# Performance work log

Hardware: AMD Instinct MI355X
Metric: run time of the kernel (lower is better)

## Reference

```python
import jax, jax.numpy as jnp
import numpy as np

SEQ, BATCH, HIDDEN, HEADS = 2048, 2, 1024, 16
HEAD_DIM = HIDDEN // HEADS
NORM = float(np.sqrt(HEAD_DIM))
NEG_MIN = float(np.finfo(np.float32).min)


def setup_inputs() -> dict:
    key = jax.random.key(0)
    ks = jax.random.split(key, 9)
    xavier = lambda k: (jax.random.normal(k, (HIDDEN, HIDDEN), jnp.float32)
                        * np.sqrt(2.0 / (HIDDEN + HIDDEN)))
    hidden_states = jax.random.normal(ks[0], (SEQ, BATCH, HIDDEN), jnp.float32)
    # causal (left-to-right) bool mask, True = attend
    attention_mask = jnp.tril(jnp.ones((SEQ, SEQ), dtype=bool))[None, None, :, :]
    return {
        "hidden_states": hidden_states,
        "attention_mask": attention_mask,
        "Wq": xavier(ks[1]), "bq": jnp.zeros((HIDDEN,), jnp.float32),
        "Wk": xavier(ks[2]), "bk": jnp.zeros((HIDDEN,), jnp.float32),
        "Wv": xavier(ks[3]), "bv": jnp.zeros((HIDDEN,), jnp.float32),
        "Wo": xavier(ks[4]), "bo": jnp.zeros((HIDDEN,), jnp.float32),
    }


def reference(hidden_states, attention_mask, Wq, bq, Wk, bk, Wv, bv, Wo, bo):
    s, b, _ = hidden_states.shape
    # projections (F.linear: x @ W.T + b), seq-first layout -> [s,b,h,d]
    q = (hidden_states @ Wq.T + bq).reshape(s, b, HEADS, HEAD_DIM) / NORM
    k = (hidden_states @ Wk.T + bk).reshape(s, b, HEADS, HEAD_DIM)
    v = (hidden_states @ Wv.T + bv).reshape(s, b, HEADS, HEAD_DIM)
    # scores [b,h,q,k] (Q already pre-scaled by 1/sqrt(d))
    scores = jnp.einsum("qbhd,kbhd->bhqk", q, k)
    scores = jnp.where(attention_mask, scores, NEG_MIN)
    probs = jax.nn.softmax(scores, axis=-1)
    # context [b,h,q,d] -> permute(2,0,1,3) -> [q,b,h,d] -> [q,b,hidden]
    ctx = jnp.einsum("bhqk,kbhd->qbhd", probs, v).reshape(s, b, HIDDEN)
    return ctx @ Wo.T + bo
```

## Files before the change

kernel.cpp:

```cpp
#include <hip/hip_runtime.h>
#include <hip/hip_bf16.h>
#include <cstdint>
#include <math.h>

#define SEQ 2048
#define BATCH 2
#define HID 1024
#define NH 16
#define HD 64
#define MROWS (SEQ * BATCH)

typedef __attribute__((ext_vector_type(8))) short bf16x8;
typedef __attribute__((ext_vector_type(4))) float f32x4;

typedef const __attribute__((address_space(1))) void* gas_t;
typedef __attribute__((address_space(3))) void* las_t;

static __device__ __forceinline__ unsigned short f2bf(float x) {
    __hip_bfloat16 h = __float2bfloat16(x);
    unsigned short u;
    __builtin_memcpy(&u, &h, 2);
    return u;
}

__global__ __launch_bounds__(256) void f2bf_kern(const float* __restrict__ in,
                                                 unsigned short* __restrict__ out,
                                                 int n8) {
    int i = blockIdx.x * 256 + threadIdx.x;
    if (i >= n8) return;
    const float4* p = (const float4*)in + (size_t)i * 2;
    float4 a = p[0], b = p[1];
    union { unsigned short us[8]; uint4 v; } o;
    o.us[0] = f2bf(a.x); o.us[1] = f2bf(a.y); o.us[2] = f2bf(a.z); o.us[3] = f2bf(a.w);
    o.us[4] = f2bf(b.x); o.us[5] = f2bf(b.y); o.us[6] = f2bf(b.z); o.us[7] = f2bf(b.w);
    ((uint4*)out)[i] = o.v;
}

#define GBK 32

template <int BNT2>
__global__ __launch_bounds__(256) void gemm_bf16(
    const unsigned short* __restrict__ A, const unsigned short* __restrict__ W,
    const float* __restrict__ b0, const float* __restrict__ b1,
    const float* __restrict__ b2,
    unsigned short* __restrict__ Qo, unsigned short* __restrict__ Ko,
    unsigned short* __restrict__ Vo, float* __restrict__ Fo, int mode) {
    constexpr int BN = BNT2 * 32;
    __shared__ unsigned short As[2][128 * GBK];
    __shared__ unsigned short Bs[2][BN * GBK];
    const int t = threadIdx.x;
    const int lane = t & 63, w = t >> 6;
    const int wr = w & 1, wc = w >> 1;
    const int m0 = blockIdx.x * 128, n0 = blockIdx.y * BN;

    f32x4 acc[4][BNT2];
#pragma unroll
    for (int i = 0; i < 4; ++i)
#pragma unroll
        for (int j = 0; j < BNT2; ++j) acc[i][j] = {0.f, 0.f, 0.f, 0.f};

    const unsigned short* gA = A + (size_t)(m0 + w * 16 + (lane >> 2)) * HID + (lane & 3) * 8;
    const unsigned short* gB = W + (size_t)(n0 + w * 16 + (lane >> 2)) * HID + (lane & 3) * 8;

    auto stage = [&](int buf, int k0) {
#pragma unroll
        for (int c = 0; c < 2; ++c)
            __builtin_amdgcn_global_load_lds((gas_t)(gA + (size_t)c * 64 * HID + k0),
                                             (las_t)(&As[buf][(c * 64 + w * 16) * GBK]), 16, 0, 0);
#pragma unroll
        for (int c = 0; c < BN / 64; ++c)
            __builtin_amdgcn_global_load_lds((gas_t)(gB + (size_t)c * 64 * HID + k0),
                                             (las_t)(&Bs[buf][(c * 64 + w * 16) * GBK]), 16, 0, 0);
    };

    const int arow = wr * 64 + (lane & 15);
    const int brow = wc * (BNT2 * 16) + (lane & 15);
    const int kfo = (lane >> 4) * 8;

    stage(0, 0);
    int cur = 0;
    for (int k0 = 0; k0 < HID; k0 += GBK) {
        __syncthreads();
        if (k0 + GBK < HID) stage(cur ^ 1, k0 + GBK);
        bf16x8 af[4], bfr[BNT2];
#pragma unroll
        for (int mt = 0; mt < 4; ++mt)
            af[mt] = *(const bf16x8*)(&As[cur][(arow + mt * 16) * GBK + kfo]);
#pragma unroll
        for (int nt = 0; nt < BNT2; ++nt)
            bfr[nt] = *(const bf16x8*)(&Bs[cur][(brow + nt * 16) * GBK + kfo]);
#pragma unroll
        for (int mt = 0; mt < 4; ++mt)
#pragma unroll
            for (int nt = 0; nt < BNT2; ++nt)
                acc[mt][nt] = __builtin_amdgcn_mfma_f32_16x16x32_bf16(
                    af[mt], bfr[nt], acc[mt][nt], 0, 0, 0);
        cur ^= 1;
    }

    const int seg = n0 >> 10;
    const float* bias = (mode == 1) ? b0 : (seg == 0 ? b0 : (seg == 1 ? b1 : b2));
    const float scale = (mode == 0 && seg == 0) ? 0.125f : 1.0f;
    const int nbase = (n0 & 1023) + wc * (BNT2 * 16);

    float bvals[BNT2];
#pragma unroll
    for (int nt = 0; nt < BNT2; ++nt)
        bvals[nt] = bias[nbase + nt * 16 + (lane & 15)];

#pragma unroll
    for (int mt = 0; mt < 4; ++mt)
#pragma unroll
        for (int nt = 0; nt < BNT2; ++nt)
#pragma unroll
            for (int i = 0; i < 4; ++i) {
                float v = (acc[mt][nt][i] + bvals[nt]) * scale;
                int m = m0 + wr * 64 + mt * 16 + (lane >> 4) * 4 + i;
                int n = nbase + nt * 16 + (lane & 15);
                if (mode == 1) {
                    Fo[(size_t)m * HID + n] = v;
                } else if (seg == 0) {
                    Qo[(size_t)m * HID + n] = f2bf(v);
                } else if (seg == 1) {
                    Ko[(size_t)m * HID + n] = f2bf(v);
                } else {
                    Vo[(size_t)n * MROWS + (m & 1) * SEQ + (m >> 1)] = f2bf(v);
                }
            }
}

__global__ __launch_bounds__(256) void attn_mfma(const unsigned short* __restrict__ Qb,
                                                 const unsigned short* __restrict__ Kb,
                                                 const unsigned short* __restrict__ Vt,
                                                 unsigned short* __restrict__ Ob) {
    __shared__ unsigned short Kl[2][64 * 64];
    __shared__ unsigned short Vl[2][64 * 64];
    __shared__ unsigned short QP[64 * 64];

    const int t = threadIdx.x;
    const int lane = t & 63, w = t >> 6;

    const int flat = (int)blockIdx.x + (int)blockIdx.y * 32;
    const int xcd = flat & 7, ii = flat >> 3;
    const int bh = xcd * 4 + (ii >> 5);
    const int qt = 31 - (ii & 31);
    const int b = bh >> 4, h = bh & 15;
    const int q0 = qt * 64;

    const int lrow_base = w * 8 + (lane >> 3);
    const int chunkb = (lane & 7) * 16;

    auto stage_kv = [&](int buf, int kt) {
        const int k0 = kt * 64;
#pragma unroll
        for (int c = 0; c < 2; ++c) {
            int lr = c * 32 + lrow_base;
            int sb = chunkb ^ ((lr & 7) << 4);
            const unsigned short* ksrc =
                Kb + ((size_t)(k0 + lr) * 2 + b) * HID + h * 64 + (sb >> 1);
            const unsigned short* vsrc =
                Vt + (size_t)(h * 64 + lr) * MROWS + b * SEQ + k0 + (sb >> 1);
            __builtin_amdgcn_global_load_lds((gas_t)ksrc,
                (las_t)(&Kl[buf][(c * 32 + w * 8) * 64]), 16, 0, 0);
            __builtin_amdgcn_global_load_lds((gas_t)vsrc,
                (las_t)(&Vl[buf][(c * 32 + w * 8) * 64]), 16, 0, 0);
        }
    };

    stage_kv(0, 0);

#pragma unroll
    for (int c = 0; c < 2; ++c) {
        int f = c * 256 + t;
        int r = f >> 3, dc = f & 7;
        uint4 v = *(const uint4*)(Qb + (size_t)((q0 + r) * 2 + b) * HID + h * 64 + dc * 8);
        *(uint4*)((char*)QP + r * 128 + ((dc * 16) ^ ((r & 7) << 4))) = v;
    }

    f32x4 acc[4];
#pragma unroll
    for (int nt = 0; nt < 4; ++nt) acc[nt] = {0.f, 0.f, 0.f, 0.f};
    float mrow[4] = {-INFINITY, -INFINITY, -INFINITY, -INFINITY};
    float lrow[4] = {0.f, 0.f, 0.f, 0.f};
    bf16x8 qf[2];

    int cur = 0;
    for (int kt = 0; kt <= qt; ++kt) {
        __syncthreads();
        if (kt < qt) stage_kv(cur ^ 1, kt + 1);
        if (kt == 0) {
            int r = w * 16 + (lane & 15);
            int base = r * 128, sw = (r & 7) << 4;
            qf[0] = *(const bf16x8*)((char*)QP + base + ((((lane >> 4) * 16) + 0) ^ sw));
            qf[1] = *(const bf16x8*)((char*)QP + base + ((((lane >> 4) * 16) + 64) ^ sw));
        }
        const char* Kc = (const char*)Kl[cur];
        const char* Vc = (const char*)Vl[cur];

        f32x4 s[4];
#pragma unroll
        for (int ct = 0; ct < 4; ++ct) {
            int j = ct * 16 + (lane & 15);
            int base = j * 128, sw = (j & 7) << 4;
            bf16x8 kf0 = *(const bf16x8*)(Kc + base + ((((lane >> 4) * 16) + 0) ^ sw));
            bf16x8 kf1 = *(const bf16x8*)(Kc + base + ((((lane >> 4) * 16) + 64) ^ sw));
            f32x4 z = {0.f, 0.f, 0.f, 0.f};
            z = __builtin_amdgcn_mfma_f32_16x16x32_bf16(qf[0], kf0, z, 0, 0, 0);
            z = __builtin_amdgcn_mfma_f32_16x16x32_bf16(qf[1], kf1, z, 0, 0, 0);
            s[ct] = z;
        }

        if (kt == qt) {
#pragma unroll
            for (int ct = 0; ct < 4; ++ct) {
                int j = ct * 16 + (lane & 15);
#pragma unroll
                for (int i = 0; i < 4; ++i) {
                    int q = w * 16 + (lane >> 4) * 4 + i;
                    if (j > q) s[ct][i] = -3.0e38f;
                }
            }
        }

#pragma unroll
        for (int i = 0; i < 4; ++i) {
            float mx = fmaxf(fmaxf(s[0][i], s[1][i]), fmaxf(s[2][i], s[3][i]));
            mx = fmaxf(mx, __shfl_xor(mx, 1));
            mx = fmaxf(mx, __shfl_xor(mx, 2));
            mx = fmaxf(mx, __shfl_xor(mx, 4));
            mx = fmaxf(mx, __shfl_xor(mx, 8));
            float mn = fmaxf(mrow[i], mx);
            float corr = __expf(mrow[i] - mn);
            mrow[i] = mn;
            float rs = 0.f;
#pragma unroll
            for (int ct = 0; ct < 4; ++ct) {
                float pe = __expf(s[ct][i] - mn);
                s[ct][i] = pe;
                rs += pe;
            }
            rs += __shfl_xor(rs, 1);
            rs += __shfl_xor(rs, 2);
            rs += __shfl_xor(rs, 4);
            rs += __shfl_xor(rs, 8);
            lrow[i] = lrow[i] * corr + rs;
#pragma unroll
            for (int nt = 0; nt < 4; ++nt) acc[nt][i] *= corr;
        }

#pragma unroll
        for (int ct = 0; ct < 4; ++ct)
#pragma unroll
            for (int i = 0; i < 4; ++i) {
                int r = w * 16 + (lane >> 4) * 4 + i;
                int jb = (ct * 16 + (lane & 15)) * 2;
                *(unsigned short*)((char*)QP + r * 128 + (jb ^ ((r & 7) << 4))) = f2bf(s[ct][i]);
            }
        asm volatile("s_waitcnt lgkmcnt(0)" ::: "memory");
        __builtin_amdgcn_sched_barrier(0);

        bf16x8 pf[2];
        {
            int r = w * 16 + (lane & 15);
            int base = r * 128, sw = (r & 7) << 4;
            pf[0] = *(const bf16x8*)((char*)QP + base + ((((lane >> 4) * 16) + 0) ^ sw));
            pf[1] = *(const bf16x8*)((char*)QP + base + ((((lane >> 4) * 16) + 64) ^ sw));
        }
#pragma unroll
        for (int nt = 0; nt < 4; ++nt) {
            int d = nt * 16 + (lane & 15);
            int base = d * 128, sw = (d & 7) << 4;
            bf16x8 v0 = *(const bf16x8*)(Vc + base + ((((lane >> 4) * 16) + 0) ^ sw));
            bf16x8 v1 = *(const bf16x8*)(Vc + base + ((((lane >> 4) * 16) + 64) ^ sw));
            acc[nt] = __builtin_amdgcn_mfma_f32_16x16x32_bf16(pf[0], v0, acc[nt], 0, 0, 0);
            acc[nt] = __builtin_amdgcn_mfma_f32_16x16x32_bf16(pf[1], v1, acc[nt], 0, 0, 0);
        }
        cur ^= 1;
    }

#pragma unroll
    for (int i = 0; i < 4; ++i) {
        float inv = 1.0f / lrow[i];
        int q = q0 + w * 16 + (lane >> 4) * 4 + i;
#pragma unroll
        for (int nt = 0; nt < 4; ++nt) {
            int col = h * 64 + nt * 16 + (lane & 15);
            Ob[(size_t)(q * 2 + b) * HID + col] = f2bf(acc[nt][i] * inv);
        }
    }
}

extern "C" void kernel_launch(void* const* d_in, const int* in_sizes, int n_in,
                              void* d_out, int out_size, void* d_ws, size_t ws_size,
                              hipStream_t stream) {
    const float* hs = (const float*)d_in[0];
    const float* Wq = (const float*)d_in[2];
    const float* bq = (const float*)d_in[3];
    const float* Wk = (const float*)d_in[4];
    const float* bk = (const float*)d_in[5];
    const float* Wv = (const float*)d_in[6];
    const float* bv = (const float*)d_in[7];
    const float* Wo = (const float*)d_in[8];
    const float* bo = (const float*)d_in[9];

    char* ws = (char*)d_ws;
    unsigned short* hs_bf   = (unsigned short*)(ws);
    unsigned short* Wqkv_bf = (unsigned short*)(ws + (8u << 20));
    unsigned short* Wo_bf   = (unsigned short*)(ws + (14u << 20));
    unsigned short* Q_bf    = (unsigned short*)(ws + (16u << 20));
    unsigned short* K_bf    = (unsigned short*)(ws + (24u << 20));
    unsigned short* Vt_bf   = (unsigned short*)(ws + (32u << 20));
    unsigned short* ctx_bf  = (unsigned short*)(ws + (40u << 20));

    dim3 blk(256);
    const int WN8 = HID * HID / 8;
    hipLaunchKernelGGL(f2bf_kern, dim3(MROWS * HID / 8 / 256), blk, 0, stream, hs, hs_bf, MROWS * HID / 8);
    hipLaunchKernelGGL(f2bf_kern, dim3(WN8 / 256), blk, 0, stream, Wq, Wqkv_bf, WN8);
    hipLaunchKernelGGL(f2bf_kern, dim3(WN8 / 256), blk, 0, stream, Wk, Wqkv_bf + (size_t)HID * HID, WN8);
    hipLaunchKernelGGL(f2bf_kern, dim3(WN8 / 256), blk, 0, stream, Wv, Wqkv_bf + (size_t)2 * HID * HID, WN8);
    hipLaunchKernelGGL(f2bf_kern, dim3(WN8 / 256), blk, 0, stream, Wo, Wo_bf, WN8);

    hipLaunchKernelGGL((gemm_bf16<4>), dim3(MROWS / 128, 24), blk, 0, stream,
                       hs_bf, Wqkv_bf, bq, bk, bv, Q_bf, K_bf, Vt_bf, (float*)nullptr, 0);

    hipLaunchKernelGGL(attn_mfma, dim3(32, 32), blk, 0, stream,
                       Q_bf, K_bf, Vt_bf, ctx_bf);

    hipLaunchKernelGGL((gemm_bf16<2>), dim3(MROWS / 128, 16), blk, 0, stream,
                       ctx_bf, Wo_bf, bo, bo, bo,
                       (unsigned short*)nullptr, (unsigned short*)nullptr,
                       (unsigned short*)nullptr, (float*)d_out, 1);
}
```

Measured before the change: 274.6 us.

## Triple-buffer GEMM with vmcnt waits, XCD-aware remap, and pair causal attention tiles

The GEMM moves from double to triple buffering with explicit vmcnt waits and raw barriers, so two tiles of loads stay in flight while MFMAs run. Its block index is also remapped so that blocks sharing weight columns land on the same XCD, for better L2 reuse. The attention kernel now gives each block two query tiles (qt and 31-qt), which balances causal work per block and halves the grid. The costs are more LDS per GEMM block and fewer attention blocks, which may lower occupancy and parallelism.

```diff
diff --git a/kernel.cpp b/kernel.cpp
--- a/kernel.cpp
+++ b/kernel.cpp
@@ -37,6 +37,7 @@
 }
 
 #define GBK 32
+#define NT (HID / GBK)
 
 template <int BNT2>
 __global__ __launch_bounds__(256) void gemm_bf16(
@@ -46,12 +47,19 @@
     unsigned short* __restrict__ Qo, unsigned short* __restrict__ Ko,
     unsigned short* __restrict__ Vo, float* __restrict__ Fo, int mode) {
     constexpr int BN = BNT2 * 32;
-    __shared__ unsigned short As[2][128 * GBK];
-    __shared__ unsigned short Bs[2][BN * GBK];
+    constexpr int LOADS = 2 + BN / 64;
+    __shared__ unsigned short As[3][128 * GBK];
+    __shared__ unsigned short Bs[3][BN * GBK];
     const int t = threadIdx.x;
     const int lane = t & 63, w = t >> 6;
     const int wr = w & 1, wc = w >> 1;
-    const int m0 = blockIdx.x * 128, n0 = blockIdx.y * BN;
+
+    const int d = (int)blockIdx.x + (int)blockIdx.y * (int)gridDim.x;
+    const int ppx = (int)gridDim.y >> 3;
+    const int xcd = d & 7, slot = d >> 3;
+    const int by = xcd * ppx + (slot >> 5);
+    const int bx = slot & 31;
+    const int m0 = bx * 128, n0 = by * BN;
 
     f32x4 acc[4][BNT2];
 #pragma unroll
@@ -62,7 +70,8 @@
     const unsigned short* gA = A + (size_t)(m0 + w * 16 + (lane >> 2)) * HID + (lane & 3) * 8;
     const unsigned short* gB = W + (size_t)(n0 + w * 16 + (lane >> 2)) * HID + (lane & 3) * 8;
 
-    auto stage = [&](int buf, int k0) {
+    auto stage = [&](int buf, int kt) {
+        const int k0 = kt * GBK;
 #pragma unroll
         for (int c = 0; c < 2; ++c)
             __builtin_amdgcn_global_load_lds((gas_t)(gA + (size_t)c * 64 * HID + k0),
@@ -77,25 +86,36 @@
     const int brow = wc * (BNT2 * 16) + (lane & 15);
     const int kfo = (lane >> 4) * 8;
 
-    stage(0, 0);
-    int cur = 0;
-    for (int k0 = 0; k0 < HID; k0 += GBK) {
-        __syncthreads();
-        if (k0 + GBK < HID) stage(cur ^ 1, k0 + GBK);
+    stage(0, 0); stage(1, 1); stage(2, 2);
+    int bn = 0;
+    for (int kt = 0; kt < NT; ++kt) {
+        if (kt <= NT - 3)
+            asm volatile("s_waitcnt vmcnt(%0)" :: "n"(2 * LOADS) : "memory");
+        else if (kt == NT - 2)
+            asm volatile("s_waitcnt vmcnt(%0)" :: "n"(LOADS) : "memory");
+        else
+            asm volatile("s_waitcnt vmcnt(0)" ::: "memory");
+        __builtin_amdgcn_s_barrier();
+
         bf16x8 af[4], bfr[BNT2];
 #pragma unroll
         for (int mt = 0; mt < 4; ++mt)
-            af[mt] = *(const bf16x8*)(&As[cur][(arow + mt * 16) * GBK + kfo]);
+            af[mt] = *(const bf16x8*)(&As[bn][(arow + mt * 16) * GBK + kfo]);
 #pragma unroll
         for (int nt = 0; nt < BNT2; ++nt)
-            bfr[nt] = *(const bf16x8*)(&Bs[cur][(brow + nt * 16) * GBK + kfo]);
+            bfr[nt] = *(const bf16x8*)(&Bs[bn][(brow + nt * 16) * GBK + kfo]);
 #pragma unroll
         for (int mt = 0; mt < 4; ++mt)
 #pragma unroll
             for (int nt = 0; nt < BNT2; ++nt)
                 acc[mt][nt] = __builtin_amdgcn_mfma_f32_16x16x32_bf16(
                     af[mt], bfr[nt], acc[mt][nt], 0, 0, 0);
-        cur ^= 1;
+
+        asm volatile("s_waitcnt lgkmcnt(0)" ::: "memory");
+        __builtin_amdgcn_sched_barrier(0);
+        __builtin_amdgcn_s_barrier();
+        if (kt + 3 < NT) stage(bn, kt + 3);
+        bn = (bn == 2) ? 0 : bn + 1;
     }
 
     const int seg = n0 >> 10;
@@ -140,152 +160,157 @@
     const int t = threadIdx.x;
     const int lane = t & 63, w = t >> 6;
 
-    const int flat = (int)blockIdx.x + (int)blockIdx.y * 32;
+    const int flat = (int)blockIdx.x + (int)blockIdx.y * 16;
     const int xcd = flat & 7, ii = flat >> 3;
-    const int bh = xcd * 4 + (ii >> 5);
-    const int qt = 31 - (ii & 31);
+    const int bh = xcd * 4 + (ii >> 4);
+    const int p = ii & 15;
     const int b = bh >> 4, h = bh & 15;
-    const int q0 = qt * 64;
 
     const int lrow_base = w * 8 + (lane >> 3);
     const int chunkb = (lane & 7) * 16;
 
-    auto stage_kv = [&](int buf, int kt) {
-        const int k0 = kt * 64;
+    for (int pass = 0; pass < 2; ++pass) {
+        const int qt = pass == 0 ? (31 - p) : p;
+        const int q0 = qt * 64;
+        if (pass) __syncthreads();
+
+        auto stage_kv = [&](int buf, int kt) {
+            const int k0 = kt * 64;
+#pragma unroll
+            for (int c = 0; c < 2; ++c) {
+                int lr = c * 32 + lrow_base;
+                int sb = chunkb ^ ((lr & 7) << 4);
+                const unsigned short* ksrc =
+                    Kb + ((size_t)(k0 + lr) * 2 + b) * HID + h * 64 + (sb >> 1);
+                const unsigned short* vsrc =
+                    Vt + (size_t)(h * 64 + lr) * MROWS + b * SEQ + k0 + (sb >> 1);
+                __builtin_amdgcn_global_load_lds((gas_t)ksrc,
+                    (las_t)(&Kl[buf][(c * 32 + w * 8) * 64]), 16, 0, 0);
+                __builtin_amdgcn_global_load_lds((gas_t)vsrc,
+                    (las_t)(&Vl[buf][(c * 32 + w * 8) * 64]), 16, 0, 0);
+            }
+        };
+
+        stage_kv(0, 0);
+
 #pragma unroll
         for (int c = 0; c < 2; ++c) {
-            int lr = c * 32 + lrow_base;
-            int sb = chunkb ^ ((lr & 7) << 4);
-            const unsigned short* ksrc =
-                Kb + ((size_t)(k0 + lr) * 2 + b) * HID + h * 64 + (sb >> 1);
-            const unsigned short* vsrc =
-                Vt + (size_t)(h * 64 + lr) * MROWS + b * SEQ + k0 + (sb >> 1);
-            __builtin_amdgcn_global_load_lds((gas_t)ksrc,
-                (las_t)(&Kl[buf][(c * 32 + w * 8) * 64]), 16, 0, 0);
-            __builtin_amdgcn_global_load_lds((gas_t)vsrc,
-                (las_t)(&Vl[buf][(c * 32 + w * 8) * 64]), 16, 0, 0);
+            int f = c * 256 + t;
+            int r = f >> 3, dc = f & 7;
+            uint4 v = *(const uint4*)(Qb + (size_t)((q0 + r) * 2 + b) * HID + h * 64 + dc * 8);
+            *(uint4*)((char*)QP + r * 128 + ((dc * 16) ^ ((r & 7) << 4))) = v;
         }
-    };
-
-    stage_kv(0, 0);
-
-#pragma unroll
-    for (int c = 0; c < 2; ++c) {
-        int f = c * 256 + t;
-        int r = f >> 3, dc = f & 7;
-        uint4 v = *(const uint4*)(Qb + (size_t)((q0 + r) * 2 + b) * HID + h * 64 + dc * 8);
-        *(uint4*)((char*)QP + r * 128 + ((dc * 16) ^ ((r & 7) << 4))) = v;
-    }
-
-    f32x4 acc[4];
-#pragma unroll
-    for (int nt = 0; nt < 4; ++nt) acc[nt] = {0.f, 0.f, 0.f, 0.f};
-    float mrow[4] = {-INFINITY, -INFINITY, -INFINITY, -INFINITY};
-    float lrow[4] = {0.f, 0.f, 0.f, 0.f};
-    bf16x8 qf[2];
-
-    int cur = 0;
-    for (int kt = 0; kt <= qt; ++kt) {
-        __syncthreads();
-        if (kt < qt) stage_kv(cur ^ 1, kt + 1);
-        if (kt == 0) {
-            int r = w * 16 + (lane & 15);
-            int base = r * 128, sw = (r & 7) << 4;
-            qf[0] = *(const bf16x8*)((char*)QP + base + ((((lane >> 4) * 16) + 0) ^ sw));
-            qf[1] = *(const bf16x8*)((char*)QP + base + ((((lane >> 4) * 16) + 64) ^ sw));
-        }
-        const char* Kc = (const char*)Kl[cur];
-        const char* Vc = (const char*)Vl[cur];
-
-        f32x4 s[4];
-#pragma unroll
-        for (int ct = 0; ct < 4; ++ct) {
-            int j = ct * 16 + (lane & 15);
-            int base = j * 128, sw = (j & 7) << 4;
-            bf16x8 kf0 = *(const bf16x8*)(Kc + base + ((((lane >> 4) * 16) + 0) ^ sw));
-            bf16x8 kf1 = *(const bf16x8*)(Kc + base + ((((lane >> 4) * 16) + 64) ^ sw));
-            f32x4 z = {0.f, 0.f, 0.f, 0.f};
-            z = __builtin_amdgcn_mfma_f32_16x16x32_bf16(qf[0], kf0, z, 0, 0, 0);
-            z = __builtin_amdgcn_mfma_f32_16x16x32_bf16(qf[1], kf1, z, 0, 0, 0);
-            s[ct] = z;
-        }
-
-        if (kt == qt) {
+
+        f32x4 acc[4];
+#pragma unroll
+        for (int nt = 0; nt < 4; ++nt) acc[nt] = {0.f, 0.f, 0.f, 0.f};
+        float mrow[4] = {-INFINITY, -INFINITY, -INFINITY, -INFINITY};
+        float lrow[4] = {0.f, 0.f, 0.f, 0.f};
+        bf16x8 qf[2];
+
+        int cur = 0;
+        for (int kt = 0; kt <= qt; ++kt) {
+            __syncthreads();
+            if (kt < qt) stage_kv(cur ^ 1, kt + 1);
+            if (kt == 0) {
+                int r = w * 16 + (lane & 15);
+                int base = r * 128, sw = (r & 7) << 4;
+                qf[0] = *(const bf16x8*)((char*)QP + base + ((((lane >> 4) * 16) + 0) ^ sw));
+                qf[1] = *(const bf16x8*)((char*)QP + base + ((((lane >> 4) * 16) + 64) ^ sw));
+            }
+            const char* Kc = (const char*)Kl[cur];
+            const char* Vc = (const char*)Vl[cur];
+
+            f32x4 s[4];
 #pragma unroll
             for (int ct = 0; ct < 4; ++ct) {
                 int j = ct * 16 + (lane & 15);
+                int base = j * 128, sw = (j & 7) << 4;
+                bf16x8 kf0 = *(const bf16x8*)(Kc + base + ((((lane >> 4) * 16) + 0) ^ sw));
+                bf16x8 kf1 = *(const bf16x8*)(Kc + base + ((((lane >> 4) * 16) + 64) ^ sw));
+                f32x4 z = {0.f, 0.f, 0.f, 0.f};
+                z = __builtin_amdgcn_mfma_f32_16x16x32_bf16(qf[0], kf0, z, 0, 0, 0);
+                z = __builtin_amdgcn_mfma_f32_16x16x32_bf16(qf[1], kf1, z, 0, 0, 0);
+                s[ct] = z;
+            }
+
+            if (kt == qt) {
+#pragma unroll
+                for (int ct = 0; ct < 4; ++ct) {
+                    int j = ct * 16 + (lane & 15);
+#pragma unroll
+                    for (int i = 0; i < 4; ++i) {
+                        int q = w * 16 + (lane >> 4) * 4 + i;
+                        if (j > q) s[ct][i] = -3.0e38f;
+                    }
+                }
+            }
+
+#pragma unroll
+            for (int i = 0; i < 4; ++i) {
+                float mx = fmaxf(fmaxf(s[0][i], s[1][i]), fmaxf(s[2][i], s[3][i]));
+                mx = fmaxf(mx, __shfl_xor(mx, 1));
+                mx = fmaxf(mx, __shfl_xor(mx, 2));
+                mx = fmaxf(mx, __shfl_xor(mx, 4));
+                mx = fmaxf(mx, __shfl_xor(mx, 8));
+                float mn = fmaxf(mrow[i], mx);
+                float corr = __expf(mrow[i] - mn);
+                mrow[i] = mn;
+                float rs = 0.f;
+#pragma unroll
+                for (int ct = 0; ct < 4; ++ct) {
+                    float pe = __expf(s[ct][i] - mn);
+                    s[ct][i] = pe;
+                    rs += pe;
+                }
+                rs += __shfl_xor(rs, 1);
+                rs += __shfl_xor(rs, 2);
+                rs += __shfl_xor(rs, 4);
+                rs += __shfl_xor(rs, 8);
+                lrow[i] = lrow[i] * corr + rs;
+#pragma unroll
+                for (int nt = 0; nt < 4; ++nt) acc[nt][i] *= corr;
+            }
+
+#pragma unroll
+            for (int ct = 0; ct < 4; ++ct)
 #pragma unroll
                 for (int i = 0; i < 4; ++i) {
-                    int q = w * 16 + (lane >> 4) * 4 + i;
-                    if (j > q) s[ct][i] = -3.0e38f;
+                    int r = w * 16 + (lane >> 4) * 4 + i;
+                    int jb = (ct * 16 + (lane & 15)) * 2;
+                    *(unsigned short*)((char*)QP + r * 128 + (jb ^ ((r & 7) << 4))) = f2bf(s[ct][i]);
                 }
-            }
+            asm volatile("s_waitcnt lgkmcnt(0)" ::: "memory");
+            __builtin_amdgcn_sched_barrier(0);
+
+            bf16x8 pf[2];
+            {
+                int r = w * 16 + (lane & 15);
+                int base = r * 128, sw = (r & 7) << 4;
+                pf[0] = *(const bf16x8*)((char*)QP + base + ((((lane >> 4) * 16) + 0) ^ sw));
+                pf[1] = *(const bf16x8*)((char*)QP + base + ((((lane >> 4) * 16) + 64) ^ sw));
+            }
+#pragma unroll
+            for (int nt = 0; nt < 4; ++nt) {
+                int dd = nt * 16 + (lane & 15);
+                int base = dd * 128, sw = (dd & 7) << 4;
+                bf16x8 v0 = *(const bf16x8*)(Vc + base + ((((lane >> 4) * 16) + 0) ^ sw));
+                bf16x8 v1 = *(const bf16x8*)(Vc + base + ((((lane >> 4) * 16) + 64) ^ sw));
+                acc[nt] = __builtin_amdgcn_mfma_f32_16x16x32_bf16(pf[0], v0, acc[nt], 0, 0, 0);
+                acc[nt] = __builtin_amdgcn_mfma_f32_16x16x32_bf16(pf[1], v1, acc[nt], 0, 0, 0);
+            }
+            cur ^= 1;
         }
 
 #pragma unroll
         for (int i = 0; i < 4; ++i) {
-            float mx = fmaxf(fmaxf(s[0][i], s[1][i]), fmaxf(s[2][i], s[3][i]));
-            mx = fmaxf(mx, __shfl_xor(mx, 1));
-            mx = fmaxf(mx, __shfl_xor(mx, 2));
-            mx = fmaxf(mx, __shfl_xor(mx, 4));
-            mx = fmaxf(mx, __shfl_xor(mx, 8));
-            float mn = fmaxf(mrow[i], mx);
-            float corr = __expf(mrow[i] - mn);
-            mrow[i] = mn;
-            float rs = 0.f;
-#pragma unroll
-            for (int ct = 0; ct < 4; ++ct) {
-                float pe = __expf(s[ct][i] - mn);
-                s[ct][i] = pe;
-                rs += pe;
-            }
-            rs += __shfl_xor(rs, 1);
-            rs += __shfl_xor(rs, 2);
-            rs += __shfl_xor(rs, 4);
-            rs += __shfl_xor(rs, 8);
-            lrow[i] = lrow[i] * corr + rs;
-#pragma unroll
-            for (int nt = 0; nt < 4; ++nt) acc[nt][i] *= corr;
-        }
-
-#pragma unroll
-        for (int ct = 0; ct < 4; ++ct)
-#pragma unroll
-            for (int i = 0; i < 4; ++i) {
-                int r = w * 16 + (lane >> 4) * 4 + i;
-                int jb = (ct * 16 + (lane & 15)) * 2;
-                *(unsigned short*)((char*)QP + r * 128 + (jb ^ ((r & 7) << 4))) = f2bf(s[ct][i]);
-            }
-        asm volatile("s_waitcnt lgkmcnt(0)" ::: "memory");
-        __builtin_amdgcn_sched_barrier(0);
-
-        bf16x8 pf[2];
-        {
-            int r = w * 16 + (lane & 15);
-            int base = r * 128, sw = (r & 7) << 4;
-            pf[0] = *(const bf16x8*)((char*)QP + base + ((((lane >> 4) * 16) + 0) ^ sw));
-            pf[1] = *(const bf16x8*)((char*)QP + base + ((((lane >> 4) * 16) + 64) ^ sw));
-        }
-#pragma unroll
-        for (int nt = 0; nt < 4; ++nt) {
-            int d = nt * 16 + (lane & 15);
-            int base = d * 128, sw = (d & 7) << 4;
-            bf16x8 v0 = *(const bf16x8*)(Vc + base + ((((lane >> 4) * 16) + 0) ^ sw));
-            bf16x8 v1 = *(const bf16x8*)(Vc + base + ((((lane >> 4) * 16) + 64) ^ sw));
-            acc[nt] = __builtin_amdgcn_mfma_f32_16x16x32_bf16(pf[0], v0, acc[nt], 0, 0, 0);
-            acc[nt] = __builtin_amdgcn_mfma_f32_16x16x32_bf16(pf[1], v1, acc[nt], 0, 0, 0);
-        }
-        cur ^= 1;
-    }
-
-#pragma unroll
-    for (int i = 0; i < 4; ++i) {
-        float inv = 1.0f / lrow[i];
-        int q = q0 + w * 16 + (lane >> 4) * 4 + i;
-#pragma unroll
-        for (int nt = 0; nt < 4; ++nt) {
-            int col = h * 64 + nt * 16 + (lane & 15);
-            Ob[(size_t)(q * 2 + b) * HID + col] = f2bf(acc[nt][i] * inv);
+            float inv = 1.0f / lrow[i];
+            int q = q0 + w * 16 + (lane >> 4) * 4 + i;
+#pragma unroll
+            for (int nt = 0; nt < 4; ++nt) {
+                int col = h * 64 + nt * 16 + (lane & 15);
+                Ob[(size_t)(q * 2 + b) * HID + col] = f2bf(acc[nt][i] * inv);
+            }
         }
     }
 }
@@ -323,7 +348,7 @@
     hipLaunchKernelGGL((gemm_bf16<4>), dim3(MROWS / 128, 24), blk, 0, stream,
                        hs_bf, Wqkv_bf, bq, bk, bv, Q_bf, K_bf, Vt_bf, (float*)nullptr, 0);
 
-    hipLaunchKernelGGL(attn_mfma, dim3(32, 32), blk, 0, stream,
+    hipLaunchKernelGGL(attn_mfma, dim3(16, 32), blk, 0, stream,
                        Q_bf, K_bf, Vt_bf, ctx_bf);
 
     hipLaunchKernelGGL((gemm_bf16<2>), dim3(MROWS / 128, 16), blk, 0, stream,
```

Measured after the change: 249.7 us. 9.1% less time.
